# Kernel tuning notes

Hardware: AMD Instinct MI355X
Metric: run time of the kernel (lower is better)

## Reference

```python
import jax, jax.numpy as jnp
import numpy as np
import math

D_MODEL = 1024
N_HEADS = 16
HEAD_DIM = D_MODEL // N_HEADS
WINDOW = 256
LN_EPS = 1e-5


def _layernorm(x, g, b):
    mu = jnp.mean(x, axis=-1, keepdims=True)
    var = jnp.var(x, axis=-1, keepdims=True)
    return (x - mu) * jax.lax.rsqrt(var + LN_EPS) * g + b


def _window_mask(L):
    # row i attends to columns [i - W//2, i + W//2] inclusive; -inf elsewhere
    i = jnp.arange(L)[:, None]
    j = jnp.arange(L)[None, :]
    inside = (j >= i - WINDOW // 2) & (j <= i + WINDOW // 2)
    return jnp.where(inside, 0.0, -jnp.inf)  # [L, L]


def setup_inputs() -> dict:
    key = jax.random.key(0)
    ks = jax.random.split(key, 6)
    B, L, D = 2, 2048, D_MODEL
    s = 0.02
    return {
        "x": jax.random.normal(ks[0], (B, L, D), jnp.float32),
        "qkv_w": jax.random.normal(ks[1], (D, 3 * D), jnp.float32) * s,
        "qkv_b": jnp.zeros((3 * D,), jnp.float32),
        "out_w": jax.random.normal(ks[2], (D, D), jnp.float32) * s,
        "out_b": jnp.zeros((D,), jnp.float32),
        "ln1_g": jnp.ones((D,), jnp.float32),
        "ln1_b": jnp.zeros((D,), jnp.float32),
        "ln2_g": jnp.ones((D,), jnp.float32),
        "ln2_b": jnp.zeros((D,), jnp.float32),
        "ffn_w1": jax.random.normal(ks[3], (D, 2 * D), jnp.float32) * s,
        "ffn_b1": jnp.zeros((2 * D,), jnp.float32),
        "ffn_w2": jax.random.normal(ks[4], (2 * D, D), jnp.float32) * s,
        "ffn_b2": jnp.zeros((D,), jnp.float32),
    }


def reference(x, qkv_w, qkv_b, out_w, out_b, ln1_g, ln1_b, ln2_g, ln2_b,
              ffn_w1, ffn_b1, ffn_w2, ffn_b2):
    B, L, D = x.shape
    # --- sparse (windowed) attention on LN1(x) ---
    h = _layernorm(x, ln1_g, ln1_b)
    qkv = h @ qkv_w + qkv_b                       # [B, L, 3D]
    qkv = qkv.reshape(B, L, 3, N_HEADS, HEAD_DIM)
    q = qkv[:, :, 0].transpose(0, 2, 1, 3)        # [B, H, L, hd]
    k = qkv[:, :, 1].transpose(0, 2, 1, 3)
    v = qkv[:, :, 2].transpose(0, 2, 1, 3)
    scores = jnp.einsum('bhqd,bhkd->bhqk', q, k) / math.sqrt(HEAD_DIM)
    scores = scores + _window_mask(L)             # broadcast [L,L] over [B,H]
    attn = jax.nn.softmax(scores, axis=-1)
    out = jnp.einsum('bhqk,bhkd->bhqd', attn, v)  # [B, H, L, hd]
    out = out.transpose(0, 2, 1, 3).reshape(B, L, D)
    attn_out = out @ out_w + out_b
    x = x + attn_out
    # --- FFN on LN2(x) ---
    h2 = _layernorm(x, ln2_g, ln2_b)
    ffn = jax.nn.gelu(h2 @ ffn_w1 + ffn_b1, approximate=False) @ ffn_w2 + ffn_b2
    return x + ffn
```

## Files before the change

### kernel.cpp

```cpp
#include <hip/hip_runtime.h>
#include <hip/hip_bf16.h>

#define D_MODEL 1024
#define L_SEQ   2048
#define BATCH   2
#define NROWS   (BATCH*L_SEQ)
#define N_HEADS 16
#define HD      64
#define WIN     128

typedef __attribute__((ext_vector_type(8))) short short8;
typedef __attribute__((ext_vector_type(4))) float f32x4;
typedef __attribute__((ext_vector_type(4))) int   i32x4;
typedef __attribute__((ext_vector_type(4))) unsigned short u16x4;

__device__ __forceinline__ float bf2f(unsigned short u) {
  union { unsigned int i; float f; } c;
  c.i = ((unsigned int)u) << 16;
  return c.f;
}
__device__ __forceinline__ unsigned short f2bf(float f) {
  __hip_bfloat16 h = __float2bfloat16(f);
  return *reinterpret_cast<unsigned short*>(&h);
}

__device__ __forceinline__ void gload16(const void* g, void* l) {
  __builtin_amdgcn_global_load_lds((const __attribute__((address_space(1))) unsigned int*)g,
                                   (__attribute__((address_space(3))) unsigned int*)l, 16, 0, 0);
}

__device__ __forceinline__ void wtrans_body(const float* __restrict__ W,
                                            __hip_bfloat16* __restrict__ Wt,
                                            int K, int N, int tile_id) {
  __shared__ float tile[32][33];
  int tx = threadIdx.x & 31, ty = threadIdx.x >> 5;
  int ntile_n = N >> 5;
  int n0 = (tile_id % ntile_n) * 32, k0 = (tile_id / ntile_n) * 32;
#pragma unroll
  for (int i = 0; i < 4; ++i) {
    int k = k0 + ty + i * 8;
    tile[ty + i * 8][tx] = W[(size_t)k * N + n0 + tx];
  }
  __syncthreads();
#pragma unroll
  for (int i = 0; i < 4; ++i) {
    int n = n0 + ty + i * 8;
    Wt[(size_t)n * K + k0 + tx] = __float2bfloat16(tile[tx][ty + i * 8]);
  }
}

__device__ __forceinline__ void ln_body(const float* __restrict__ x,
                                        const float* __restrict__ g,
                                        const float* __restrict__ beta,
                                        __hip_bfloat16* __restrict__ out, int row) {
  int t = threadIdx.x;
  const float4* xr = (const float4*)(x + (size_t)row * D_MODEL);
  float4 v = xr[t];
  float s  = v.x + v.y + v.z + v.w;
  float sq = v.x * v.x + v.y * v.y + v.z * v.z + v.w * v.w;
#pragma unroll
  for (int off = 32; off; off >>= 1) {
    s  += __shfl_xor(s, off);
    sq += __shfl_xor(sq, off);
  }
  __shared__ float red[8];
  int w = t >> 6;
  if ((t & 63) == 0) { red[w] = s; red[4 + w] = sq; }
  __syncthreads();
  s  = red[0] + red[1] + red[2] + red[3];
  sq = red[4] + red[5] + red[6] + red[7];
  float mean = s * (1.0f / 1024.0f);
  float var  = sq * (1.0f / 1024.0f) - mean * mean;
  float rs   = rsqrtf(var + 1e-5f);
  float4 gv = ((const float4*)g)[t];
  float4 bv = ((const float4*)beta)[t];
  u16x4 o;
  o.x = f2bf((v.x - mean) * rs * gv.x + bv.x);
  o.y = f2bf((v.y - mean) * rs * gv.y + bv.y);
  o.z = f2bf((v.z - mean) * rs * gv.z + bv.z);
  o.w = f2bf((v.w - mean) * rs * gv.w + bv.w);
  ((u16x4*)(out + (size_t)row * D_MODEL))[t] = o;
}

__global__ __launch_bounds__(256) void prep_kernel(
    const float* __restrict__ qkv_w, __hip_bfloat16* __restrict__ wqkvT,
    const float* __restrict__ out_w, __hip_bfloat16* __restrict__ woutT,
    const float* __restrict__ ffn_w1, __hip_bfloat16* __restrict__ wf1T,
    const float* __restrict__ ffn_w2, __hip_bfloat16* __restrict__ wf2T,
    const float* __restrict__ x, const float* __restrict__ ln1_g,
    const float* __restrict__ ln1_b, __hip_bfloat16* __restrict__ hbuf) {
  int id = blockIdx.x;
  if (id < 3072)      wtrans_body(qkv_w,  wqkvT, 1024, 3072, id);
  else if (id < 4096) wtrans_body(out_w,  woutT, 1024, 1024, id - 3072);
  else if (id < 6144) wtrans_body(ffn_w1, wf1T,  1024, 2048, id - 4096);
  else if (id < 8192) wtrans_body(ffn_w2, wf2T,  2048, 1024, id - 6144);
  else                ln_body(x, ln1_g, ln1_b, hbuf, id - 8192);
}

__global__ __launch_bounds__(256) void ln_kernel(const float* __restrict__ x,
                                                 const float* __restrict__ g,
                                                 const float* __restrict__ beta,
                                                 __hip_bfloat16* __restrict__ out) {
  ln_body(x, g, beta, out, blockIdx.x);
}

__global__ __launch_bounds__(256) void vtrans_kernel(const __hip_bfloat16* __restrict__ qkv,
                                                     __hip_bfloat16* __restrict__ vT) {
  __shared__ unsigned short tile[64][72];
  int bh = blockIdx.y, b = bh >> 4, h = bh & 15;
  int j0 = blockIdx.x * 64;
  int t = threadIdx.x;
#pragma unroll
  for (int i = 0; i < 2; ++i) {
    int c = t + i * 256;
    int row = c >> 3, off = c & 7;
    *(i32x4*)&tile[row][off * 8] =
        *(const i32x4*)&qkv[(size_t)(b * L_SEQ + j0 + row) * 3072 + 2 * D_MODEL + h * 64 + off * 8];
  }
  __syncthreads();
#pragma unroll
  for (int i = 0; i < 2; ++i) {
    int c = t + i * 256;
    int d = c >> 3, off = c & 7;
    short8 o;
#pragma unroll
    for (int e = 0; e < 8; ++e) o[e] = (short)tile[off * 8 + e][d];
    *(short8*)&vT[((size_t)bh * 64 + d) * 2048 + j0 + off * 8] = o;
  }
}

template <int MODE>
__global__ __launch_bounds__(256) void gemm_kernel(const __hip_bfloat16* __restrict__ A,
                                                   const __hip_bfloat16* __restrict__ Bt,
                                                   const float* __restrict__ bias,
                                                   const float* __restrict__ resid,
                                                   void* __restrict__ outp,
                                                   int M, int N, int K) {
  (void)M;
  __shared__ __align__(16) char lsA[2][128 * 128];
  __shared__ __align__(16) char lsB[2][128 * 128];

  int tid  = threadIdx.x;
  int lane = tid & 63;
  int wave = tid >> 6;
  int wr = wave >> 1, wc = wave & 1;
  int l15 = lane & 15, lg = lane >> 4;

  int gx = gridDim.x;
  int nwg = gx * gridDim.y;
  int flat = blockIdx.y * gx + blockIdx.x;
  int cpx = nwg >> 3;
  int sw = (flat & 7) * cpx + (flat >> 3);
  int m0 = (sw / gx) * 128;
  int n0 = (sw % gx) * 128;

  const char* Abase = (const char*)A;
  const char* Bbase = (const char*)Bt;
  size_t strideK = (size_t)K * 2;
  int KT = K >> 6;

  int srow_in  = lane >> 3;
  int scb_src  = (((lane & 7) ^ srow_in)) * 16;

  auto STAGE = [&](int buf, int kt) {
    size_t kb = (size_t)kt * 128;
#pragma unroll
    for (int i = 0; i < 4; ++i) {
      int chunk = wave * 4 + i;
      int row = chunk * 8 + srow_in;
      gload16(Abase + (size_t)(m0 + row) * strideK + kb + scb_src, lsA[buf] + chunk * 1024);
      gload16(Bbase + (size_t)(n0 + row) * strideK + kb + scb_src, lsB[buf] + chunk * 1024);
    }
  };

  f32x4 zero = {0.f, 0.f, 0.f, 0.f};
  f32x4 acc[4][4];
#pragma unroll
  for (int i = 0; i < 4; ++i)
#pragma unroll
    for (int j = 0; j < 4; ++j) acc[i][j] = zero;

  STAGE(0, 0);
  __syncthreads();

  for (int kt = 0; kt < KT; ++kt) {
    int cur = kt & 1;
    if (kt + 1 < KT) STAGE(cur ^ 1, kt + 1);
#pragma unroll
    for (int ks = 0; ks < 2; ++ks) {
      short8 af[4], bfr[4];
#pragma unroll
      for (int mi = 0; mi < 4; ++mi) {
        int row = wr * 64 + mi * 16 + l15;
        af[mi] = *(const short8*)(lsA[cur] + row * 128 + ((ks * 64 + lg * 16) ^ ((row & 7) << 4)));
      }
#pragma unroll
      for (int ni = 0; ni < 4; ++ni) {
        int row = wc * 64 + ni * 16 + l15;
        bfr[ni] = *(const short8*)(lsB[cur] + row * 128 + ((ks * 64 + lg * 16) ^ ((row & 7) << 4)));
      }
#pragma unroll
      for (int mi = 0; mi < 4; ++mi)
#pragma unroll
        for (int ni = 0; ni < 4; ++ni)
          acc[mi][ni] = __builtin_amdgcn_mfma_f32_16x16x32_bf16(af[mi], bfr[ni], acc[mi][ni], 0, 0, 0);
    }
    __syncthreads();
  }

  int colg = n0 + wc * 64;
  int rowg = m0 + wr * 64;
#pragma unroll
  for (int mi = 0; mi < 4; ++mi) {
#pragma unroll
    for (int ni = 0; ni < 4; ++ni) {
      int col = colg + ni * 16 + l15;
      float bs = bias[col];
#pragma unroll
      for (int r = 0; r < 4; ++r) {
        int row = rowg + mi * 16 + (lg << 2) + r;
        float v = acc[mi][ni][r] + bs;
        if (MODE == 1) v = 0.5f * v * (1.0f + erff(v * 0.70710678118654752f));
        if (MODE == 2) {
          ((float*)outp)[(size_t)row * N + col] = v + resid[(size_t)row * N + col];
        } else {
          ((__hip_bfloat16*)outp)[(size_t)row * N + col] = __float2bfloat16(v);
        }
      }
    }
  }
}

__global__ __launch_bounds__(256) void attn_mfma_kernel(const __hip_bfloat16* __restrict__ qkv,
                                                        const __hip_bfloat16* __restrict__ vT,
                                                        __hip_bfloat16* __restrict__ out) {
  __shared__ char Ks[2][8192];
  __shared__ char Vs[2][8192];
  __shared__ char Ps[4][2304];

  const int t = threadIdx.x;
  const int lane = t & 63;
  const int wave = t >> 6;
  const int l15 = lane & 15;
  const int lg  = lane >> 4;
  const int bh = blockIdx.y, b = bh >> 4, h = bh & 15;
  const int q0 = blockIdx.x * 64;
  const int jlo = q0 - 128;

  short8 qf0, qf1;
  {
    int qrow = q0 + wave * 16 + l15;
    const char* qp = (const char*)qkv + 2 * ((size_t)(b * L_SEQ + qrow) * 3072 + h * 64 + 8 * lg);
    qf0 = *(const short8*)qp;
    qf1 = *(const short8*)(qp + 64);
  }

  const int srow = t >> 3;
  const int soff = (t & 7) * 16;
  const int jel  = (t & 7) * 8;

  const char* kgbase = (const char*)qkv + 2 * ((size_t)b * L_SEQ * 3072 + D_MODEL + h * 64);
  const char* vgbase = (const char*)vT + 2 * ((size_t)bh * 64 * 2048);

  f32x4 sc[5][4];
#pragma unroll
  for (int c = 0; c < 5; ++c)
#pragma unroll
    for (int tt = 0; tt < 4; ++tt) sc[c][tt] = (f32x4){0.f, 0.f, 0.f, 0.f};

  {
    i32x4 kr[2];
#pragma unroll
    for (int i = 0; i < 2; ++i) {
      int rr = srow + i * 32;
      int tok = jlo + rr; tok = tok < 0 ? 0 : (tok > 2047 ? 2047 : tok);
      kr[i] = *(const i32x4*)(kgbase + (size_t)tok * 6144 + soff);
    }
#pragma unroll
    for (int i = 0; i < 2; ++i) {
      int rr = srow + i * 32;
      *(i32x4*)(Ks[0] + rr * 128 + (soff ^ ((rr & 7) << 4))) = kr[i];
    }
  }
  __syncthreads();

#pragma unroll
  for (int c = 0; c < 5; ++c) {
    int cur = c & 1;
    i32x4 nk[2];
    if (c < 4) {
#pragma unroll
      for (int i = 0; i < 2; ++i) {
        int rr = srow + i * 32;
        int tok = jlo + (c + 1) * 64 + rr; tok = tok < 0 ? 0 : (tok > 2047 ? 2047 : tok);
        nk[i] = *(const i32x4*)(kgbase + (size_t)tok * 6144 + soff);
      }
    }
#pragma unroll
    for (int tt = 0; tt < 4; ++tt) {
      int row = tt * 16 + l15;
      short8 k0 = *(const short8*)(Ks[cur] + row * 128 + ((lg * 16) ^ ((row & 7) << 4)));
      short8 k1 = *(const short8*)(Ks[cur] + row * 128 + ((64 + lg * 16) ^ ((row & 7) << 4)));
      sc[c][tt] = __builtin_amdgcn_mfma_f32_16x16x32_bf16(qf0, k0, sc[c][tt], 0, 0, 0);
      sc[c][tt] = __builtin_amdgcn_mfma_f32_16x16x32_bf16(qf1, k1, sc[c][tt], 0, 0, 0);
    }
    if (c < 4) {
      __syncthreads();
#pragma unroll
      for (int i = 0; i < 2; ++i) {
        int rr = srow + i * 32;
        *(i32x4*)(Ks[cur ^ 1] + rr * 128 + (soff ^ ((rr & 7) << 4))) = nk[i];
      }
      __syncthreads();
    }
  }

  const int iqb = q0 + wave * 16 + 4 * lg;
  const int kgb = jlo + l15;
#pragma unroll
  for (int c = 0; c < 5; ++c)
#pragma unroll
    for (int tt = 0; tt < 4; ++tt) {
      int kg = kgb + c * 64 + tt * 16;
#pragma unroll
      for (int r = 0; r < 4; ++r) {
        int iq = iqb + r;
        bool ok = (kg >= 0) && (kg < L_SEQ) && (kg >= iq - WIN) && (kg <= iq + WIN);
        sc[c][tt][r] = ok ? sc[c][tt][r] * 0.125f : -1e30f;
      }
    }
  float mx[4] = {-1e30f, -1e30f, -1e30f, -1e30f};
#pragma unroll
  for (int c = 0; c < 5; ++c)
#pragma unroll
    for (int tt = 0; tt < 4; ++tt)
#pragma unroll
      for (int r = 0; r < 4; ++r) mx[r] = fmaxf(mx[r], sc[c][tt][r]);
#pragma unroll
  for (int r = 0; r < 4; ++r)
#pragma unroll
    for (int off = 8; off; off >>= 1) mx[r] = fmaxf(mx[r], __shfl_xor(mx[r], off, 16));
  float sm[4] = {0.f, 0.f, 0.f, 0.f};
#pragma unroll
  for (int c = 0; c < 5; ++c)
#pragma unroll
    for (int tt = 0; tt < 4; ++tt)
#pragma unroll
      for (int r = 0; r < 4; ++r) {
        float p = __expf(sc[c][tt][r] - mx[r]);
        sc[c][tt][r] = p;
        sm[r] += p;
      }
#pragma unroll
  for (int r = 0; r < 4; ++r)
#pragma unroll
    for (int off = 8; off; off >>= 1) sm[r] += __shfl_xor(sm[r], off, 16);
  float inv[4];
#pragma unroll
  for (int r = 0; r < 4; ++r) inv[r] = 1.f / sm[r];
#pragma unroll
  for (int c = 0; c < 5; ++c)
#pragma unroll
    for (int tt = 0; tt < 4; ++tt)
#pragma unroll
      for (int r = 0; r < 4; ++r) sc[c][tt][r] *= inv[r];

  f32x4 o[4];
#pragma unroll
  for (int dt = 0; dt < 4; ++dt) o[dt] = (f32x4){0.f, 0.f, 0.f, 0.f};

  {
    i32x4 vr[2];
#pragma unroll
    for (int i = 0; i < 2; ++i) {
      int rr = srow + i * 32;
      int js = jlo + jel; js = js < 0 ? 0 : (js > 2040 ? 2040 : js);
      vr[i] = *(const i32x4*)(vgbase + 2 * ((size_t)rr * 2048 + js));
    }
    __syncthreads();
#pragma unroll
    for (int i = 0; i < 2; ++i) {
      int rr = srow + i * 32;
      *(i32x4*)(Vs[0] + rr * 128 + (soff ^ ((rr & 7) << 4))) = vr[i];
    }
  }
  __syncthreads();

  char* pw = Ps[wave];
#pragma unroll
  for (int c = 0; c < 5; ++c) {
    int cur = c & 1;
    i32x4 nv[2];
    if (c < 4) {
#pragma unroll
      for (int i = 0; i < 2; ++i) {
        int rr = srow + i * 32;
        int js = jlo + (c + 1) * 64 + jel; js = js < 0 ? 0 : (js > 2040 ? 2040 : js);
        nv[i] = *(const i32x4*)(vgbase + 2 * ((size_t)rr * 2048 + js));
      }
    }
#pragma unroll
    for (int tt = 0; tt < 4; ++tt)
#pragma unroll
      for (int r = 0; r < 4; ++r)
        *(unsigned short*)(pw + (4 * lg + r) * 144 + (tt * 16 + l15) * 2) = f2bf(sc[c][tt][r]);
    short8 pa0 = *(const short8*)(pw + l15 * 144 + lg * 16);
    short8 pa1 = *(const short8*)(pw + l15 * 144 + 64 + lg * 16);
#pragma unroll
    for (int dt = 0; dt < 4; ++dt) {
      int row = dt * 16 + l15;
      short8 v0 = *(const short8*)(Vs[cur] + row * 128 + ((lg * 16) ^ ((row & 7) << 4)));
      short8 v1 = *(const short8*)(Vs[cur] + row * 128 + ((64 + lg * 16) ^ ((row & 7) << 4)));
      o[dt] = __builtin_amdgcn_mfma_f32_16x16x32_bf16(pa0, v0, o[dt], 0, 0, 0);
      o[dt] = __builtin_amdgcn_mfma_f32_16x16x32_bf16(pa1, v1, o[dt], 0, 0, 0);
    }
    if (c < 4) {
      __syncthreads();
#pragma unroll
      for (int i = 0; i < 2; ++i) {
        int rr = srow + i * 32;
        *(i32x4*)(Vs[cur ^ 1] + rr * 128 + (soff ^ ((rr & 7) << 4))) = nv[i];
      }
      __syncthreads();
    }
  }

  char* ob = (char*)out + 2 * ((size_t)(b * L_SEQ + q0 + wave * 16) * D_MODEL + h * 64);
#pragma unroll
  for (int dt = 0; dt < 4; ++dt)
#pragma unroll
    for (int r = 0; r < 4; ++r)
      *(unsigned short*)(ob + 2 * ((size_t)(4 * lg + r) * D_MODEL + dt * 16 + l15)) = f2bf(o[dt][r]);
}

extern "C" void kernel_launch(void* const* d_in, const int* in_sizes, int n_in,
                              void* d_out, int out_size, void* d_ws, size_t ws_size,
                              hipStream_t stream) {
  const float* x      = (const float*)d_in[0];
  const float* qkv_w  = (const float*)d_in[1];
  const float* qkv_b  = (const float*)d_in[2];
  const float* out_w  = (const float*)d_in[3];
  const float* out_b  = (const float*)d_in[4];
  const float* ln1_g  = (const float*)d_in[5];
  const float* ln1_b  = (const float*)d_in[6];
  const float* ln2_g  = (const float*)d_in[7];
  const float* ln2_b  = (const float*)d_in[8];
  const float* ffn_w1 = (const float*)d_in[9];
  const float* ffn_b1 = (const float*)d_in[10];
  const float* ffn_w2 = (const float*)d_in[11];
  const float* ffn_b2 = (const float*)d_in[12];
  float* out = (float*)d_out;
  (void)in_sizes; (void)n_in; (void)out_size; (void)ws_size;

  char* ws = (char*)d_ws;
  size_t off = 0;
  auto alloc = [&](size_t bytes) {
    char* p = ws + off;
    off += (bytes + 255) & ~(size_t)255;
    return p;
  };
  __hip_bfloat16* hbuf    = (__hip_bfloat16*)alloc((size_t)NROWS * 1024 * 2);
  __hip_bfloat16* qkvbuf  = (__hip_bfloat16*)alloc((size_t)NROWS * 3072 * 2);
  __hip_bfloat16* attnbuf = (__hip_bfloat16*)alloc((size_t)NROWS * 1024 * 2);
  float*          x2buf   = (float*)alloc((size_t)NROWS * 1024 * 4);
  __hip_bfloat16* wqkvT   = (__hip_bfloat16*)alloc((size_t)3072 * 1024 * 2);
  __hip_bfloat16* woutT   = (__hip_bfloat16*)alloc((size_t)1024 * 1024 * 2);
  __hip_bfloat16* wf1T    = (__hip_bfloat16*)alloc((size_t)2048 * 1024 * 2);
  __hip_bfloat16* wf2T    = (__hip_bfloat16*)alloc((size_t)1024 * 2048 * 2);
  __hip_bfloat16* vTbuf   = (__hip_bfloat16*)alloc((size_t)32 * 64 * 2048 * 2);
  __hip_bfloat16* gbuf    = qkvbuf;

  dim3 blk(256);
  prep_kernel<<<8192 + NROWS, blk, 0, stream>>>(qkv_w, wqkvT, out_w, woutT,
                                                ffn_w1, wf1T, ffn_w2, wf2T,
                                                x, ln1_g, ln1_b, hbuf);
  gemm_kernel<0><<<dim3(3072 / 128, NROWS / 128), blk, 0, stream>>>(hbuf, wqkvT, qkv_b, nullptr, qkvbuf, NROWS, 3072, 1024);
  vtrans_kernel<<<dim3(L_SEQ / 64, BATCH * N_HEADS), blk, 0, stream>>>(qkvbuf, vTbuf);
  attn_mfma_kernel<<<dim3(L_SEQ / 64, BATCH * N_HEADS), blk, 0, stream>>>(qkvbuf, vTbuf, attnbuf);
  gemm_kernel<2><<<dim3(1024 / 128, NROWS / 128), blk, 0, stream>>>(attnbuf, woutT, out_b, x, x2buf, NROWS, 1024, 1024);
  ln_kernel<<<NROWS, blk, 0, stream>>>(x2buf, ln2_g, ln2_b, hbuf);
  gemm_kernel<1><<<dim3(2048 / 128, NROWS / 128), blk, 0, stream>>>(hbuf, wf1T, ffn_b1, nullptr, gbuf, NROWS, 2048, 1024);
  gemm_kernel<2><<<dim3(1024 / 128, NROWS / 128), blk, 0, stream>>>(gbuf, wf2T, ffn_b2, x2buf, out, NROWS, 1024, 2048);
}
```

Measured before the change: 273.5 us.

## Add 256x256-tile 512-thread GEMM for QKV and FFN1 projections

```diff
diff --git a/kernel.cpp b/kernel.cpp
--- a/kernel.cpp
+++ b/kernel.cpp
@@ -130,6 +130,103 @@
 }
 
 template <int MODE>
+__global__ __launch_bounds__(512, 1) void gemm256_kernel(const __hip_bfloat16* __restrict__ A,
+                                                         const __hip_bfloat16* __restrict__ Bt,
+                                                         const float* __restrict__ bias,
+                                                         void* __restrict__ outp,
+                                                         int M, int N, int K) {
+  (void)M;
+  extern __shared__ __align__(16) char lds[];
+
+  int tid  = threadIdx.x;
+  int lane = tid & 63;
+  int wave = tid >> 6;
+  int wr = wave >> 2, wc = wave & 3;
+  int l15 = lane & 15, lg = lane >> 4;
+
+  int gx = gridDim.x;
+  int nwg = gx * gridDim.y;
+  int flat = blockIdx.y * gx + blockIdx.x;
+  int cpx = nwg >> 3;
+  int sw = (flat & 7) * cpx + (flat >> 3);
+  int m0 = (sw / gx) * 256;
+  int n0 = (sw % gx) * 256;
+
+  const char* Abase = (const char*)A;
+  const char* Bbase = (const char*)Bt;
+  size_t strideK = (size_t)K * 2;
+  int KT = K >> 6;
+
+  int srow_in = lane >> 3;
+  int scb_src = ((lane & 7) ^ srow_in) * 16;
+
+  auto STAGE = [&](int buf, int kt) {
+    size_t kb = (size_t)kt * 128;
+    char* lA = lds + buf * 65536;
+    char* lB = lds + buf * 65536 + 32768;
+#pragma unroll
+    for (int i = 0; i < 4; ++i) {
+      int chunk = wave * 4 + i;
+      int row = chunk * 8 + srow_in;
+      gload16(Abase + (size_t)(m0 + row) * strideK + kb + scb_src, lA + chunk * 1024);
+      gload16(Bbase + (size_t)(n0 + row) * strideK + kb + scb_src, lB + chunk * 1024);
+    }
+  };
+
+  f32x4 acc[8][4];
+#pragma unroll
+  for (int i = 0; i < 8; ++i)
+#pragma unroll
+    for (int j = 0; j < 4; ++j) acc[i][j] = (f32x4){0.f, 0.f, 0.f, 0.f};
+
+  STAGE(0, 0);
+  __syncthreads();
+
+  for (int kt = 0; kt < KT; ++kt) {
+    int cur = kt & 1;
+    if (kt + 1 < KT) STAGE(cur ^ 1, kt + 1);
+    const char* lA = lds + cur * 65536;
+    const char* lB = lds + cur * 65536 + 32768;
+#pragma unroll
+    for (int ks = 0; ks < 2; ++ks) {
+      short8 bfr[4];
+#pragma unroll
+      for (int ni = 0; ni < 4; ++ni) {
+        int row = wc * 64 + ni * 16 + l15;
+        bfr[ni] = *(const short8*)(lB + row * 128 + ((ks * 64 + lg * 16) ^ ((row & 7) << 4)));
+      }
+#pragma unroll
+      for (int mi = 0; mi < 8; ++mi) {
+        int row = wr * 128 + mi * 16 + l15;
+        short8 af = *(const short8*)(lA + row * 128 + ((ks * 64 + lg * 16) ^ ((row & 7) << 4)));
+#pragma unroll
+        for (int ni = 0; ni < 4; ++ni)
+          acc[mi][ni] = __builtin_amdgcn_mfma_f32_16x16x32_bf16(af, bfr[ni], acc[mi][ni], 0, 0, 0);
+      }
+    }
+    __syncthreads();
+  }
+
+  int colg = n0 + wc * 64;
+  int rowg = m0 + wr * 128;
+#pragma unroll
+  for (int mi = 0; mi < 8; ++mi) {
+#pragma unroll
+    for (int ni = 0; ni < 4; ++ni) {
+      int col = colg + ni * 16 + l15;
+      float bs = bias[col];
+#pragma unroll
+      for (int r = 0; r < 4; ++r) {
+        int row = rowg + mi * 16 + (lg << 2) + r;
+        float v = acc[mi][ni][r] + bs;
+        if (MODE == 1) v = 0.5f * v * (1.0f + erff(v * 0.70710678118654752f));
+        ((__hip_bfloat16*)outp)[(size_t)row * N + col] = __float2bfloat16(v);
+      }
+    }
+  }
+}
+
+template <int MODE>
 __global__ __launch_bounds__(256) void gemm_kernel(const __hip_bfloat16* __restrict__ A,
                                                    const __hip_bfloat16* __restrict__ Bt,
                                                    const float* __restrict__ bias,
@@ -173,12 +270,11 @@
     }
   };
 
-  f32x4 zero = {0.f, 0.f, 0.f, 0.f};
   f32x4 acc[4][4];
 #pragma unroll
   for (int i = 0; i < 4; ++i)
 #pragma unroll
-    for (int j = 0; j < 4; ++j) acc[i][j] = zero;
+    for (int j = 0; j < 4; ++j) acc[i][j] = (f32x4){0.f, 0.f, 0.f, 0.f};
 
   STAGE(0, 0);
   __syncthreads();
@@ -470,15 +566,18 @@
   __hip_bfloat16* vTbuf   = (__hip_bfloat16*)alloc((size_t)32 * 64 * 2048 * 2);
   __hip_bfloat16* gbuf    = qkvbuf;
 
+  hipFuncSetAttribute((const void*)gemm256_kernel<0>, hipFuncAttributeMaxDynamicSharedMemorySize, 131072);
+  hipFuncSetAttribute((const void*)gemm256_kernel<1>, hipFuncAttributeMaxDynamicSharedMemorySize, 131072);
+
   dim3 blk(256);
   prep_kernel<<<8192 + NROWS, blk, 0, stream>>>(qkv_w, wqkvT, out_w, woutT,
                                                 ffn_w1, wf1T, ffn_w2, wf2T,
                                                 x, ln1_g, ln1_b, hbuf);
-  gemm_kernel<0><<<dim3(3072 / 128, NROWS / 128), blk, 0, stream>>>(hbuf, wqkvT, qkv_b, nullptr, qkvbuf, NROWS, 3072, 1024);
+  gemm256_kernel<0><<<dim3(3072 / 256, NROWS / 256), 512, 131072, stream>>>(hbuf, wqkvT, qkv_b, qkvbuf, NROWS, 3072, 1024);
   vtrans_kernel<<<dim3(L_SEQ / 64, BATCH * N_HEADS), blk, 0, stream>>>(qkvbuf, vTbuf);
   attn_mfma_kernel<<<dim3(L_SEQ / 64, BATCH * N_HEADS), blk, 0, stream>>>(qkvbuf, vTbuf, attnbuf);
   gemm_kernel<2><<<dim3(1024 / 128, NROWS / 128), blk, 0, stream>>>(attnbuf, woutT, out_b, x, x2buf, NROWS, 1024, 1024);
   ln_kernel<<<NROWS, blk, 0, stream>>>(x2buf, ln2_g, ln2_b, hbuf);
-  gemm_kernel<1><<<dim3(2048 / 128, NROWS / 128), blk, 0, stream>>>(hbuf, wf1T, ffn_b1, nullptr, gbuf, NROWS, 2048, 1024);
+  gemm256_kernel<1><<<dim3(2048 / 256, NROWS / 256), 512, 131072, stream>>>(hbuf, wf1T, ffn_b1, gbuf, NROWS, 2048, 1024);
   gemm_kernel<2><<<dim3(1024 / 128, NROWS / 128), blk, 0, stream>>>(gbuf, wf2T, ffn_b2, x2buf, out, NROWS, 1024, 2048);
 }
```

Result: slower. 281.0 us (+2.7%).
